# Kernel tuning notes

Hardware: AMD Instinct MI355X
Metric: run time of the kernel (lower is better)

Reference implementation:

```python
import jax, jax.numpy as jnp
import numpy as np

N = 50000   # nodes
E = 800000  # edges
C = 64      # channels per head (= n_channel)
H = 2       # heads
EPS = 1e-5


def _layernorm(x, g, b):
    m = jnp.mean(x, axis=-1, keepdims=True)
    v = jnp.mean((x - m) ** 2, axis=-1, keepdims=True)
    return (x - m) / jnp.sqrt(v + EPS) * g + b


def setup_inputs() -> dict:
    key = jax.random.key(0)
    ks = jax.random.split(key, 20)
    r = lambda k, shape: (jax.random.normal(k, shape, jnp.float32) * 0.05)
    inp = {
        "x": jax.random.normal(ks[0], (N, C), jnp.float32),
        "edge_index": jax.random.randint(ks[1], (2, E), 0, N, jnp.int64),
        "edge_attr": jax.random.normal(ks[2], (E, 1), jnp.float32),
        # TransformerConv params (PyG): lin_query/key/value: in=C -> H*C with bias
        "Wq": r(ks[3], (H * C, C)), "bq": r(ks[4], (H * C,)),
        "Wk": r(ks[5], (H * C, C)), "bk": r(ks[6], (H * C,)),
        "Wv": r(ks[7], (H * C, C)), "bv": r(ks[8], (H * C,)),
        # lin_edge: edge_dim=1 -> H*C, no bias
        "We": r(ks[9], (H * C, 1)),
        # lin_skip (root weight, concat=False -> out=C), with bias
        "Wskip": r(ks[10], (C, C)), "bskip": r(ks[11], (C,)),
        # shell linear + layernorms
        "Wl": r(ks[12], (C, C)), "bl": r(ks[13], (C,)),
        "g0": jnp.ones((C,), jnp.float32), "b0": jnp.zeros((C,), jnp.float32),
        "g1": jnp.ones((C,), jnp.float32), "b1": jnp.zeros((C,), jnp.float32),
    }
    return inp


def _transformer_conv(x, src, dst, edge_attr, Wq, bq, Wk, bk, Wv, bv, We, Wskip, bskip):
    q = (x @ Wq.T + bq).reshape(N, H, C)
    k = (x @ Wk.T + bk).reshape(N, H, C)
    v = (x @ Wv.T + bv).reshape(N, H, C)
    e = (edge_attr @ We.T).reshape(E, H, C)        # [E,H,C]
    k_j = k[src] + e                               # gather + edge key
    v_j = v[src] + e
    alpha = jnp.einsum('ehc,ehc->eh', q[dst], k_j) / jnp.sqrt(jnp.float32(C))
    # segment softmax over destination nodes
    amax = jax.ops.segment_max(alpha, dst, num_segments=N)      # [N,H]
    ex = jnp.exp(alpha - amax[dst])
    denom = jax.ops.segment_sum(ex, dst, num_segments=N)        # [N,H]
    w = ex / denom[dst]                                          # [E,H]
    out = jax.ops.segment_sum(v_j * w[..., None], dst, num_segments=N)  # [N,H,C]
    out = out.mean(axis=1)                                       # concat=False -> mean heads
    return out + x @ Wskip.T + bskip                             # root weight skip


def reference(x, edge_index, edge_attr, Wq, bq, Wk, bk, Wv, bv, We, Wskip, bskip,
              Wl, bl, g0, b0, g1, b1):
    src, dst = edge_index[0], edge_index[1]
    h = _transformer_conv(x, src, dst, edge_attr, Wq, bq, Wk, bk, Wv, bv, We, Wskip, bskip)
    x = x + _layernorm(h, g0, b0)
    x = x + _layernorm(x @ Wl.T + bl, g1, b1)
    return x
```

## Files before the change

kernel.cpp:

```cpp
#include <hip/hip_runtime.h>
#include <hip/hip_fp16.h>

#define NN 50000
#define NE 800000

typedef unsigned short u16;
typedef float v2f __attribute__((ext_vector_type(2)));
typedef short bf16x8 __attribute__((ext_vector_type(8)));
typedef float f32x4 __attribute__((ext_vector_type(4)));

template <int CTRL>
__device__ __forceinline__ float dpp_add(float p) {
  const int v = __builtin_amdgcn_update_dpp(0, __float_as_int(p), CTRL, 0xF, 0xF, true);
  return p + __int_as_float(v);
}
__device__ __forceinline__ float red16(float p) {
  p = dpp_add<0xB1>(p);
  p = dpp_add<0x4E>(p);
  p = dpp_add<0x141>(p);
  p = dpp_add<0x140>(p);
  return p;
}

__device__ __forceinline__ unsigned short f2bf(float f) {
  unsigned u = __float_as_uint(f);
  return (unsigned short)((u + 0x7FFFu + ((u >> 16) & 1u)) >> 16);
}
__device__ __forceinline__ unsigned pk2(float a, float b) {
  return (unsigned)f2bf(a) | ((unsigned)f2bf(b) << 16);
}

__global__ __launch_bounds__(256) void k_gemm_qkv(
    const float* __restrict__ x,
    const float* __restrict__ Wq, const float* __restrict__ bq,
    const float* __restrict__ Wk, const float* __restrict__ bk,
    const float* __restrict__ Wv, const float* __restrict__ bv,
    const float* __restrict__ Wskip, const float* __restrict__ bskip,
    const int* __restrict__ ei, int* __restrict__ cnt, int* __restrict__ pos,
    float* __restrict__ qs, unsigned* __restrict__ kvp, float* __restrict__ skip)
{
  const int t = threadIdx.x;

  if (blockIdx.y == 1) {
    const int e0 = blockIdx.x * 1024 + t;
    #pragma unroll
    for (int it = 0; it < 4; it++) {
      const int e = e0 + it * 256;
      if (e < NE) pos[e] = atomicAdd(&cnt[ei[NE + e]], 1);
    }
    return;
  }

  __shared__ unsigned short xb[64][72];
  __shared__ unsigned short wb[64][72];
  __shared__ float cb[64][68];
  const int tileN = blockIdx.x * 64;

  {
    const int nl = t >> 2, c0 = (t & 3) * 16;
    const int n = tileN + nl;
    float4 a0, a1, a2, a3;
    if (n < NN) {
      const float4* xr = (const float4*)(x + (size_t)n * 64 + c0);
      a0 = xr[0]; a1 = xr[1]; a2 = xr[2]; a3 = xr[3];
    } else {
      a0 = a1 = a2 = a3 = make_float4(0.f, 0.f, 0.f, 0.f);
    }
    *(uint4*)&xb[nl][c0] =
        make_uint4(pk2(a0.x, a0.y), pk2(a0.z, a0.w), pk2(a1.x, a1.y), pk2(a1.z, a1.w));
    *(uint4*)&xb[nl][c0 + 8] =
        make_uint4(pk2(a2.x, a2.y), pk2(a2.z, a2.w), pk2(a3.x, a3.y), pk2(a3.z, a3.w));
  }

  const int w = t >> 6;
  const int l = t & 63;
  const int rb = w * 16;
  const int frow = l & 15;
  const int fk = (l >> 4) * 8;

  const bf16x8 a0 = *(const bf16x8*)&xb[rb + frow][fk];
  const bf16x8 a1 = *(const bf16x8*)&xb[rb + frow][fk + 32];

  for (int s = 0; s < 7; s++) {
    const float* Wb; const float* bias; int cbase; int kind;
    switch (s) {
      case 0: Wb = Wq;    bias = bq;    cbase = 0;  kind = 0; break;
      case 1: Wb = Wq;    bias = bq;    cbase = 64; kind = 0; break;
      case 2: Wb = Wk;    bias = bk;    cbase = 0;  kind = 2; break;
      case 3: Wb = Wv;    bias = bv;    cbase = 0;  kind = 3; break;
      case 4: Wb = Wk;    bias = bk;    cbase = 64; kind = 2; break;
      case 5: Wb = Wv;    bias = bv;    cbase = 64; kind = 3; break;
      default: Wb = Wskip; bias = bskip; cbase = 0; kind = 1; break;
    }

    __syncthreads();
    {
      const int nl = t >> 2, c0 = (t & 3) * 16;
      const float4* wr = (const float4*)(Wb + (size_t)(cbase + nl) * 64 + c0);
      float4 b0 = wr[0], b1 = wr[1], b2 = wr[2], b3 = wr[3];
      *(uint4*)&wb[nl][c0] =
          make_uint4(pk2(b0.x, b0.y), pk2(b0.z, b0.w), pk2(b1.x, b1.y), pk2(b1.z, b1.w));
      *(uint4*)&wb[nl][c0 + 8] =
          make_uint4(pk2(b2.x, b2.y), pk2(b2.z, b2.w), pk2(b3.x, b3.y), pk2(b3.z, b3.w));
    }
    __syncthreads();

    #pragma unroll
    for (int ct = 0; ct < 4; ct++) {
      const bf16x8 b0 = *(const bf16x8*)&wb[ct * 16 + frow][fk];
      const bf16x8 b1 = *(const bf16x8*)&wb[ct * 16 + frow][fk + 32];
      f32x4 acc = {0.f, 0.f, 0.f, 0.f};
      acc = __builtin_amdgcn_mfma_f32_16x16x32_bf16(a0, b0, acc, 0, 0, 0);
      acc = __builtin_amdgcn_mfma_f32_16x16x32_bf16(a1, b1, acc, 0, 0, 0);
      const int col = ct * 16 + frow;
      const int row0 = rb + ((l >> 4) << 2);
      const float bb = bias[cbase * (kind != 1 ? 1 : 0) + col];
      if (kind == 0) {
        #pragma unroll
        for (int j = 0; j < 4; j++) {
          const int n = tileN + row0 + j;
          if (n < NN) qs[(size_t)n * 128 + cbase + col] = acc[j] + bb;
        }
      } else if (kind == 1) {
        #pragma unroll
        for (int j = 0; j < 4; j++) {
          const int n = tileN + row0 + j;
          if (n < NN) skip[(size_t)n * 64 + col] = acc[j] + bb;
        }
      } else {
        #pragma unroll
        for (int j = 0; j < 4; j++) cb[row0 + j][col] = acc[j] + bb;
      }
    }

    if (kind >= 2) {
      const int rrow = rb + (l >> 2);
      const int chb = (l & 3) * 16;
      const int n = tileN + rrow;
      if (n < NN) {
        const float4* c4 = (const float4*)&cb[rrow][chb];
        const float4 c0_ = c4[0], c1_ = c4[1], c2_ = c4[2], c3_ = c4[3];
        unsigned p0 = 0, p1 = 0, p2 = 0, p3 = 0;
        p0 = __builtin_amdgcn_cvt_pk_fp8_f32(c0_.x, c0_.y, p0, false);
        p0 = __builtin_amdgcn_cvt_pk_fp8_f32(c0_.z, c0_.w, p0, true);
        p1 = __builtin_amdgcn_cvt_pk_fp8_f32(c1_.x, c1_.y, p1, false);
        p1 = __builtin_amdgcn_cvt_pk_fp8_f32(c1_.z, c1_.w, p1, true);
        p2 = __builtin_amdgcn_cvt_pk_fp8_f32(c2_.x, c2_.y, p2, false);
        p2 = __builtin_amdgcn_cvt_pk_fp8_f32(c2_.z, c2_.w, p2, true);
        p3 = __builtin_amdgcn_cvt_pk_fp8_f32(c3_.x, c3_.y, p3, false);
        p3 = __builtin_amdgcn_cvt_pk_fp8_f32(c3_.z, c3_.w, p3, true);
        const int ebase = (cbase + chb) >> 2;
        unsigned* dstp = kvp + (size_t)n * 64 + ebase * 2 + ((kind == 3) ? 1 : 0);
        dstp[0] = p0; dstp[2] = p1; dstp[4] = p2; dstp[6] = p3;
      }
    }
  }
}

__global__ __launch_bounds__(1024) void k_scan(
    const int* __restrict__ cnt, int* __restrict__ rowptr) {
  __shared__ int wsum[16];
  __shared__ int boff_s;
  const int t = threadIdx.x, lane = t & 63, wid = t >> 6;
  const int b = blockIdx.x;

  {
    int pre = 0;
    for (int j = t; j < b * 1024; j += 1024) pre += cnt[j];
    #pragma unroll
    for (int m = 1; m <= 32; m <<= 1) pre += __shfl_xor(pre, m);
    if (lane == 0) wsum[wid] = pre;
    __syncthreads();
    if (t == 0) {
      int s = 0;
      #pragma unroll
      for (int j = 0; j < 16; j++) s += wsum[j];
      boff_s = s;
    }
    __syncthreads();
  }

  const int i = b * 1024 + t;
  const int val = (i < NN) ? cnt[i] : 0;
  int incl = val;
  #pragma unroll
  for (int off = 1; off < 64; off <<= 1) {
    int n = __shfl_up(incl, off, 64);
    if (lane >= off) incl += n;
  }
  if (lane == 63) wsum[wid] = incl;
  __syncthreads();
  if (t < 16) {
    int wv = wsum[t];
    int wincl = wv;
    #pragma unroll
    for (int off = 1; off < 16; off <<= 1) {
      int n = __shfl_up(wincl, off, 64);
      if (t >= off) wincl += n;
    }
    wsum[t] = wincl - wv;
  }
  __syncthreads();
  if (i < NN) rowptr[i] = boff_s + wsum[wid] + incl - val;
  if (b == 0 && t == 0) rowptr[NN] = NE;
}

__global__ __launch_bounds__(256) void k_fill(
    const int* __restrict__ ei, const float* __restrict__ ea,
    const int* __restrict__ rowptr, const int* __restrict__ pos,
    unsigned* __restrict__ epk) {
  const int e = blockIdx.x * 256 + threadIdx.x;
  if (e < NE) {
    const int dst = ei[NE + e];
    const int idx = rowptr[dst] + pos[e];
    const unsigned rec = (unsigned)ei[e] |
        ((unsigned)__half_as_ushort(__float2half_rn(ea[e])) << 16);
    epk[idx] = rec;
  }
}

__global__ __launch_bounds__(256) void k_fused(
    const float* __restrict__ qs, const unsigned* __restrict__ kvp,
    const float* __restrict__ skip, const float* __restrict__ x,
    const int* __restrict__ rowptr, const unsigned* __restrict__ epk,
    const float* __restrict__ We,
    const float* __restrict__ Wl, const float* __restrict__ bl,
    const float* __restrict__ g0, const float* __restrict__ b0,
    const float* __restrict__ g1, const float* __restrict__ b1,
    float* __restrict__ out)
{
  __shared__ float wlT[64][65];
  __shared__ float scx[4][64];
  const int t = threadIdx.x;
  {
    const int jl = t >> 2, c0 = (t & 3) * 16;
    const float4* wr = (const float4*)(Wl + (size_t)jl * 64 + c0);
    float4 w0 = wr[0], w1 = wr[1], w2 = wr[2], w3 = wr[3];
    wlT[c0 +  0][jl] = w0.x; wlT[c0 +  1][jl] = w0.y; wlT[c0 +  2][jl] = w0.z; wlT[c0 +  3][jl] = w0.w;
    wlT[c0 +  4][jl] = w1.x; wlT[c0 +  5][jl] = w1.y; wlT[c0 +  6][jl] = w1.z; wlT[c0 +  7][jl] = w1.w;
    wlT[c0 +  8][jl] = w2.x; wlT[c0 +  9][jl] = w2.y; wlT[c0 + 10][jl] = w2.z; wlT[c0 + 11][jl] = w2.w;
    wlT[c0 + 12][jl] = w3.x; wlT[c0 + 13][jl] = w3.y; wlT[c0 + 14][jl] = w3.z; wlT[c0 + 15][jl] = w3.w;
  }
  __syncthreads();

  const int w = t >> 6;
  const int dst = __builtin_amdgcn_readfirstlane(blockIdx.x * 4 + w);
  const int lane = t & 63;
  const int half = lane >> 5;
  const int el = lane & 31;

  const float4 qv = ((const float4*)(qs + (size_t)dst * 128))[el];
  const float4 we4 = ((const float4*)We)[el];
  const float skipv = skip[(size_t)dst * 64 + lane];
  const float xv    = x[(size_t)dst * 64 + lane];

  const float qwe = red16(qv.x * we4.x + qv.y * we4.y + qv.z * we4.z + qv.w * we4.w);

  const int base = rowptr[dst];
  const int deg  = rowptr[dst + 1] - base;
  const uint2* kv8 = (const uint2*)kvp;
  const unsigned* ep = epk + base;

  float s = 0.f, sw = 0.f;
  float sv0 = 0.f, sv1 = 0.f, sv2 = 0.f, sv3 = 0.f;

  const float SCL = 0.18033688011112042f;

#define UNPACK_W(er) __half2float(__ushort_as_half((unsigned short)((er) >> 16)))
#define PROC(u, wg, mask)                                                   \
  {                                                                         \
    const v2f k01 = __builtin_amdgcn_cvt_pk_f32_fp8((u).x, false);          \
    const v2f k23 = __builtin_amdgcn_cvt_pk_f32_fp8((u).x, true);           \
    const v2f v01 = __builtin_amdgcn_cvt_pk_f32_fp8((u).y, false);          \
    const v2f v23 = __builtin_amdgcn_cvt_pk_f32_fp8((u).y, true);           \
    const float p = red16(qv.x * k01.x + qv.y * k01.y +                     \
                          qv.z * k23.x + qv.w * k23.y);                     \
    float e_ = exp2f((p + (wg) * qwe) * SCL);                               \
    e_ = (mask) ? e_ : 0.f;                                                 \
    s += e_; sw += e_ * (wg);                                               \
    sv0 += e_ * v01.x; sv1 += e_ * v01.y;                                   \
    sv2 += e_ * v23.x; sv3 += e_ * v23.y;                                   \
  }

  int i = 0;
  for (; i + 8 <= deg; i += 8) {
    const unsigned er0 = ep[i + half];
    const unsigned er1 = ep[i + 2 + half];
    const unsigned er2 = ep[i + 4 + half];
    const unsigned er3 = ep[i + 6 + half];
    const uint2 u0 = kv8[(size_t)(er0 & 0xFFFFu) * 32 + el];
    const uint2 u1 = kv8[(size_t)(er1 & 0xFFFFu) * 32 + el];
    const uint2 u2 = kv8[(size_t)(er2 & 0xFFFFu) * 32 + el];
    const uint2 u3 = kv8[(size_t)(er3 & 0xFFFFu) * 32 + el];
    PROC(u0, UNPACK_W(er0), true)
    PROC(u1, UNPACK_W(er1), true)
    PROC(u2, UNPACK_W(er2), true)
    PROC(u3, UNPACK_W(er3), true)
  }
  for (; i + 4 <= deg; i += 4) {
    const unsigned er0 = ep[i + half];
    const unsigned er1 = ep[i + 2 + half];
    const uint2 u0 = kv8[(size_t)(er0 & 0xFFFFu) * 32 + el];
    const uint2 u1 = kv8[(size_t)(er1 & 0xFFFFu) * 32 + el];
    PROC(u0, UNPACK_W(er0), true)
    PROC(u1, UNPACK_W(er1), true)
  }
  for (; i < deg; i += 2) {
    const int idx = i + half;
    const bool valid = idx < deg;
    const unsigned er = ep[valid ? idx : (deg - 1)];
    const uint2 u = kv8[(size_t)(er & 0xFFFFu) * 32 + el];
    PROC(u, UNPACK_W(er), valid)
  }
#undef PROC
#undef UNPACK_W

  s  += __shfl_xor(s, 32);
  sw += __shfl_xor(sw, 32);
  sv0 += __shfl_xor(sv0, 32); sv1 += __shfl_xor(sv1, 32);
  sv2 += __shfl_xor(sv2, 32); sv3 += __shfl_xor(sv3, 32);

  float a0 = 0.f, a1 = 0.f, a2 = 0.f, a3 = 0.f;
  if (deg > 0) {
    const float inv = 1.f / s;
    a0 = (sv0 + sw * we4.x) * inv;
    a1 = (sv1 + sw * we4.y) * inv;
    a2 = (sv2 + sw * we4.z) * inv;
    a3 = (sv3 + sw * we4.w) * inv;
  }
  a0 = 0.5f * (a0 + __shfl_xor(a0, 16));
  a1 = 0.5f * (a1 + __shfl_xor(a1, 16));
  a2 = 0.5f * (a2 + __shfl_xor(a2, 16));
  a3 = 0.5f * (a3 + __shfl_xor(a3, 16));
  if (half == 0 && el < 16) {
    ((float4*)scx[w])[el] = make_float4(a0, a1, a2, a3);
  }
  const float hv = scx[w][lane] + skipv;

  float m1 = hv, m2 = hv * hv;
  m1 = red16(m1); m2 = red16(m2);
  m1 += __shfl_xor(m1, 16); m2 += __shfl_xor(m2, 16);
  m1 += __shfl_xor(m1, 32); m2 += __shfl_xor(m2, 32);
  const float mean = m1 * (1.f / 64.f);
  const float var = fmaxf(m2 * (1.f / 64.f) - mean * mean, 0.f);
  const float x1 = xv + (hv - mean) * rsqrtf(var + 1e-5f) * g0[lane] + b0[lane];

  scx[w][lane] = x1;
  float y0 = 0.f, y1 = 0.f, y2 = 0.f, y3 = 0.f;
  #pragma unroll
  for (int kk = 0; kk < 64; kk += 4) {
    const float4 xb4 = *(const float4*)&scx[w][kk];
    y0 += xb4.x * wlT[kk][lane];
    y1 += xb4.y * wlT[kk + 1][lane];
    y2 += xb4.z * wlT[kk + 2][lane];
    y3 += xb4.w * wlT[kk + 3][lane];
  }
  const float y = bl[lane] + (y0 + y1) + (y2 + y3);

  float n1 = y, n2 = y * y;
  n1 = red16(n1); n2 = red16(n2);
  n1 += __shfl_xor(n1, 16); n2 += __shfl_xor(n2, 16);
  n1 += __shfl_xor(n1, 32); n2 += __shfl_xor(n2, 32);
  const float mean2 = n1 * (1.f / 64.f);
  const float var2 = fmaxf(n2 * (1.f / 64.f) - mean2 * mean2, 0.f);
  out[(size_t)dst * 64 + lane] = x1 + (y - mean2) * rsqrtf(var2 + 1e-5f) * g1[lane] + b1[lane];
}

extern "C" void kernel_launch(void* const* d_in, const int* in_sizes, int n_in,
                              void* d_out, int out_size, void* d_ws, size_t ws_size,
                              hipStream_t stream) {
  const float* x     = (const float*)d_in[0];
  const int*   ei    = (const int*)d_in[1];
  const float* ea    = (const float*)d_in[2];
  const float* Wq    = (const float*)d_in[3];
  const float* bq    = (const float*)d_in[4];
  const float* Wk    = (const float*)d_in[5];
  const float* bk    = (const float*)d_in[6];
  const float* Wv    = (const float*)d_in[7];
  const float* bv    = (const float*)d_in[8];
  const float* We    = (const float*)d_in[9];
  const float* Wskip = (const float*)d_in[10];
  const float* bskip = (const float*)d_in[11];
  const float* Wl    = (const float*)d_in[12];
  const float* bl    = (const float*)d_in[13];
  const float* g0    = (const float*)d_in[14];
  const float* b0    = (const float*)d_in[15];
  const float* g1    = (const float*)d_in[16];
  const float* b1    = (const float*)d_in[17];
  float* out = (float*)d_out;

  float* ws = (float*)d_ws;
  size_t off = 0;
  float* qs   = ws + off; off += (size_t)NN * 128;
  unsigned* kvp = (unsigned*)(ws + off); off += (size_t)NN * 64;
  float* skip = ws + off; off += (size_t)NN * 64;
  int* cnt    = (int*)(ws + off); off += NN;
  int* rowptr = (int*)(ws + off); off += NN + 1;
  int* pos    = (int*)(ws + off); off += NE;
  unsigned* epk = (unsigned*)(ws + off); off += NE;

  (void)hipMemsetAsync(cnt, 0, (size_t)NN * sizeof(int), stream);

  dim3 gGemm((NN + 63) / 64, 2);
  hipLaunchKernelGGL(k_gemm_qkv, gGemm, dim3(256), 0, stream,
                     x, Wq, bq, Wk, bk, Wv, bv, Wskip, bskip, ei, cnt, pos, qs, kvp, skip);
  hipLaunchKernelGGL(k_scan, dim3(49), dim3(1024), 0, stream, cnt, rowptr);
  hipLaunchKernelGGL(k_fill, dim3((NE + 255) / 256), dim3(256), 0, stream,
                     ei, ea, rowptr, pos, epk);
  hipLaunchKernelGGL(k_fused, dim3(NN / 4), dim3(256), 0, stream,
                     qs, kvp, skip, x, rowptr, epk, We,
                     Wl, bl, g0, b0, g1, b1, out);
}
```

Baseline: 141.2 us.

## Process four edges per wavefront with 16-lane groups and 16-byte K/V loads

Restructures the per-destination aggregation so each wavefront splits into four 16-lane groups, each handling one edge, instead of two 32-lane halves. Every lane now loads a uint4 (8 fp8 K and 8 fp8 V values) and reduces the q·k dot product over 8 lanes with a shorter DPP chain. The aim is to issue wider, fewer gather loads and more edges in flight per iteration, and to cut the reduction cost per edge. The cost is more accumulator registers and an extra cross-group shuffle stage, and low-degree nodes waste more lanes in the masked tail.

```diff
diff --git a/kernel.cpp b/kernel.cpp
--- a/kernel.cpp
+++ b/kernel.cpp
@@ -19,6 +19,12 @@
   p = dpp_add<0x4E>(p);
   p = dpp_add<0x141>(p);
   p = dpp_add<0x140>(p);
+  return p;
+}
+__device__ __forceinline__ float red8(float p) {
+  p = dpp_add<0xB1>(p);
+  p = dpp_add<0x4E>(p);
+  p = dpp_add<0x141>(p);
   return p;
 }
 
@@ -246,94 +252,101 @@
   const int w = t >> 6;
   const int dst = __builtin_amdgcn_readfirstlane(blockIdx.x * 4 + w);
   const int lane = t & 63;
-  const int half = lane >> 5;
-  const int el = lane & 31;
-
-  const float4 qv = ((const float4*)(qs + (size_t)dst * 128))[el];
-  const float4 we4 = ((const float4*)We)[el];
+  const int q4 = lane >> 4;
+  const int ql = lane & 15;
+
+  const float4 qv0 = ((const float4*)(qs + (size_t)dst * 128))[ql * 2];
+  const float4 qv1 = ((const float4*)(qs + (size_t)dst * 128))[ql * 2 + 1];
+  const float4 we0 = ((const float4*)We)[ql * 2];
+  const float4 we1 = ((const float4*)We)[ql * 2 + 1];
   const float skipv = skip[(size_t)dst * 64 + lane];
   const float xv    = x[(size_t)dst * 64 + lane];
 
-  const float qwe = red16(qv.x * we4.x + qv.y * we4.y + qv.z * we4.z + qv.w * we4.w);
+  const float qwe = red8(qv0.x * we0.x + qv0.y * we0.y + qv0.z * we0.z + qv0.w * we0.w +
+                         qv1.x * we1.x + qv1.y * we1.y + qv1.z * we1.z + qv1.w * we1.w);
 
   const int base = rowptr[dst];
   const int deg  = rowptr[dst + 1] - base;
-  const uint2* kv8 = (const uint2*)kvp;
+  const uint4* kv16 = (const uint4*)kvp;
   const unsigned* ep = epk + base;
 
   float s = 0.f, sw = 0.f;
   float sv0 = 0.f, sv1 = 0.f, sv2 = 0.f, sv3 = 0.f;
+  float sv4 = 0.f, sv5 = 0.f, sv6 = 0.f, sv7 = 0.f;
 
   const float SCL = 0.18033688011112042f;
 
 #define UNPACK_W(er) __half2float(__ushort_as_half((unsigned short)((er) >> 16)))
-#define PROC(u, wg, mask)                                                   \
+#define PROC4(u, wg, mask)                                                  \
   {                                                                         \
     const v2f k01 = __builtin_amdgcn_cvt_pk_f32_fp8((u).x, false);          \
     const v2f k23 = __builtin_amdgcn_cvt_pk_f32_fp8((u).x, true);           \
     const v2f v01 = __builtin_amdgcn_cvt_pk_f32_fp8((u).y, false);          \
     const v2f v23 = __builtin_amdgcn_cvt_pk_f32_fp8((u).y, true);           \
-    const float p = red16(qv.x * k01.x + qv.y * k01.y +                     \
-                          qv.z * k23.x + qv.w * k23.y);                     \
+    const v2f k45 = __builtin_amdgcn_cvt_pk_f32_fp8((u).z, false);          \
+    const v2f k67 = __builtin_amdgcn_cvt_pk_f32_fp8((u).z, true);           \
+    const v2f v45 = __builtin_amdgcn_cvt_pk_f32_fp8((u).w, false);          \
+    const v2f v67 = __builtin_amdgcn_cvt_pk_f32_fp8((u).w, true);           \
+    float p = qv0.x * k01.x + qv0.y * k01.y + qv0.z * k23.x + qv0.w * k23.y \
+            + qv1.x * k45.x + qv1.y * k45.y + qv1.z * k67.x + qv1.w * k67.y;\
+    p = red8(p);                                                            \
     float e_ = exp2f((p + (wg) * qwe) * SCL);                               \
     e_ = (mask) ? e_ : 0.f;                                                 \
     s += e_; sw += e_ * (wg);                                               \
     sv0 += e_ * v01.x; sv1 += e_ * v01.y;                                   \
     sv2 += e_ * v23.x; sv3 += e_ * v23.y;                                   \
+    sv4 += e_ * v45.x; sv5 += e_ * v45.y;                                   \
+    sv6 += e_ * v67.x; sv7 += e_ * v67.y;                                   \
   }
 
   int i = 0;
   for (; i + 8 <= deg; i += 8) {
-    const unsigned er0 = ep[i + half];
-    const unsigned er1 = ep[i + 2 + half];
-    const unsigned er2 = ep[i + 4 + half];
-    const unsigned er3 = ep[i + 6 + half];
-    const uint2 u0 = kv8[(size_t)(er0 & 0xFFFFu) * 32 + el];
-    const uint2 u1 = kv8[(size_t)(er1 & 0xFFFFu) * 32 + el];
-    const uint2 u2 = kv8[(size_t)(er2 & 0xFFFFu) * 32 + el];
-    const uint2 u3 = kv8[(size_t)(er3 & 0xFFFFu) * 32 + el];
-    PROC(u0, UNPACK_W(er0), true)
-    PROC(u1, UNPACK_W(er1), true)
-    PROC(u2, UNPACK_W(er2), true)
-    PROC(u3, UNPACK_W(er3), true)
-  }
-  for (; i + 4 <= deg; i += 4) {
-    const unsigned er0 = ep[i + half];
-    const unsigned er1 = ep[i + 2 + half];
-    const uint2 u0 = kv8[(size_t)(er0 & 0xFFFFu) * 32 + el];
-    const uint2 u1 = kv8[(size_t)(er1 & 0xFFFFu) * 32 + el];
-    PROC(u0, UNPACK_W(er0), true)
-    PROC(u1, UNPACK_W(er1), true)
-  }
-  for (; i < deg; i += 2) {
-    const int idx = i + half;
+    const unsigned er0 = ep[i + q4];
+    const unsigned er1 = ep[i + 4 + q4];
+    const uint4 u0 = kv16[(size_t)(er0 & 0xFFFFu) * 16 + ql];
+    const uint4 u1 = kv16[(size_t)(er1 & 0xFFFFu) * 16 + ql];
+    PROC4(u0, UNPACK_W(er0), true)
+    PROC4(u1, UNPACK_W(er1), true)
+  }
+  for (; i < deg; i += 4) {
+    const int idx = i + q4;
     const bool valid = idx < deg;
     const unsigned er = ep[valid ? idx : (deg - 1)];
-    const uint2 u = kv8[(size_t)(er & 0xFFFFu) * 32 + el];
-    PROC(u, UNPACK_W(er), valid)
-  }
-#undef PROC
+    const uint4 u = kv16[(size_t)(er & 0xFFFFu) * 16 + ql];
+    PROC4(u, UNPACK_W(er), valid)
+  }
+#undef PROC4
 #undef UNPACK_W
 
-  s  += __shfl_xor(s, 32);
-  sw += __shfl_xor(sw, 32);
-  sv0 += __shfl_xor(sv0, 32); sv1 += __shfl_xor(sv1, 32);
-  sv2 += __shfl_xor(sv2, 32); sv3 += __shfl_xor(sv3, 32);
+  #pragma unroll
+  for (int m = 16; m <= 32; m <<= 1) {
+    s   += __shfl_xor(s, m);   sw  += __shfl_xor(sw, m);
+    sv0 += __shfl_xor(sv0, m); sv1 += __shfl_xor(sv1, m);
+    sv2 += __shfl_xor(sv2, m); sv3 += __shfl_xor(sv3, m);
+    sv4 += __shfl_xor(sv4, m); sv5 += __shfl_xor(sv5, m);
+    sv6 += __shfl_xor(sv6, m); sv7 += __shfl_xor(sv7, m);
+  }
 
   float a0 = 0.f, a1 = 0.f, a2 = 0.f, a3 = 0.f;
+  float a4 = 0.f, a5 = 0.f, a6 = 0.f, a7 = 0.f;
   if (deg > 0) {
     const float inv = 1.f / s;
-    a0 = (sv0 + sw * we4.x) * inv;
-    a1 = (sv1 + sw * we4.y) * inv;
-    a2 = (sv2 + sw * we4.z) * inv;
-    a3 = (sv3 + sw * we4.w) * inv;
-  }
-  a0 = 0.5f * (a0 + __shfl_xor(a0, 16));
-  a1 = 0.5f * (a1 + __shfl_xor(a1, 16));
-  a2 = 0.5f * (a2 + __shfl_xor(a2, 16));
-  a3 = 0.5f * (a3 + __shfl_xor(a3, 16));
-  if (half == 0 && el < 16) {
-    ((float4*)scx[w])[el] = make_float4(a0, a1, a2, a3);
+    a0 = (sv0 + sw * we0.x) * inv; a1 = (sv1 + sw * we0.y) * inv;
+    a2 = (sv2 + sw * we0.z) * inv; a3 = (sv3 + sw * we0.w) * inv;
+    a4 = (sv4 + sw * we1.x) * inv; a5 = (sv5 + sw * we1.y) * inv;
+    a6 = (sv6 + sw * we1.z) * inv; a7 = (sv7 + sw * we1.w) * inv;
+  }
+  a0 = 0.5f * (a0 + __shfl_xor(a0, 8));
+  a1 = 0.5f * (a1 + __shfl_xor(a1, 8));
+  a2 = 0.5f * (a2 + __shfl_xor(a2, 8));
+  a3 = 0.5f * (a3 + __shfl_xor(a3, 8));
+  a4 = 0.5f * (a4 + __shfl_xor(a4, 8));
+  a5 = 0.5f * (a5 + __shfl_xor(a5, 8));
+  a6 = 0.5f * (a6 + __shfl_xor(a6, 8));
+  a7 = 0.5f * (a7 + __shfl_xor(a7, 8));
+  if (lane < 8) {
+    ((float4*)scx[w])[lane * 2]     = make_float4(a0, a1, a2, a3);
+    ((float4*)scx[w])[lane * 2 + 1] = make_float4(a4, a5, a6, a7);
   }
   const float hv = scx[w][lane] + skipv;
 
```

Measured after the change: 147.0 us. 4.1% more time.
